# Optimization experiments

Hardware: AMD Instinct MI355X
Metric: run time of the kernel (lower is better)

Reference implementation:

```python
import jax, jax.numpy as jnp
import numpy as np

N, C, NE = 65536, 128, 10
INV_SQ2 = float(1.0 / np.sqrt(2.0))   # path weight sqrt(ir_out.dim / n_paths) * w3j, 0e outputs
INV_SQ6 = float(1.0 / np.sqrt(6.0))   # sqrt(1/2) * 1/sqrt(3) for the 1o.1o->0e dot path


def _fcn(x, weights):
    # e3nn FullyConnectedNet: no biases, fan-in normalized, silu between layers
    h = x
    for i, W in enumerate(weights):
        h = (h @ W) * float(1.0 / np.sqrt(W.shape[0]))
        if i < len(weights) - 1:
            h = jax.nn.silu(h)
    return h


def setup_inputs() -> dict:
    key = jax.random.key(0)
    ks = jax.random.split(key, 24)
    elem = jax.random.randint(ks[0], (N,), 0, NE)
    return {
        'node_feats_s': jax.random.normal(ks[1], (N, C), jnp.float32),
        'node_feats_v': jax.random.normal(ks[2], (N, C, 3), jnp.float32),
        'sc': jax.random.normal(ks[3], (N, 4 * C), jnp.float32),
        'node_attrs': jax.nn.one_hot(elem, NE, dtype=jnp.float32),
        'magmom_node_inv_feats': jax.random.normal(ks[4], (N, 16), jnp.float32),
        'magmom_node_attrs': jax.random.normal(ks[5], (N, 4), jnp.float32),
        'magmom_lenghts': jax.random.uniform(ks[6], (N, 1), jnp.float32),
        'Ws': jax.random.normal(ks[7], (NE, 5, C), jnp.float32),
        'Wv': jax.random.normal(ks[8], (NE, 4, C), jnp.float32),
        'Wc1': jax.random.normal(ks[9], (16, 64), jnp.float32),
        'Wc2': jax.random.normal(ks[10], (64, 64), jnp.float32),
        'Wc3': jax.random.normal(ks[11], (64, 64), jnp.float32),
        'Wc4': jax.random.normal(ks[12], (64, 4 * C), jnp.float32),
        'Wb1': jax.random.normal(ks[13], (16, 64), jnp.float32),
        'Wb2': jax.random.normal(ks[14], (64, 64), jnp.float32),
        'Wb3': jax.random.normal(ks[15], (64, 64), jnp.float32),
        'Wb4': jax.random.normal(ks[16], (64, C), jnp.float32),
        'exp_scaling': jnp.full((1,), 5.0, jnp.float32),
        'Wl0': jax.random.normal(ks[17], (2 * C, C), jnp.float32),
        'Wl1': jax.random.normal(ks[18], (2 * C, C), jnp.float32),
        'Wo0': jax.random.normal(ks[19], (C, C), jnp.float32),
        'Wo1': jax.random.normal(ks[20], (C, C), jnp.float32),
    }


def reference(node_feats_s, node_feats_v, sc, node_attrs, magmom_node_inv_feats,
              magmom_node_attrs, magmom_lenghts, Ws, Wv, Wc1, Wc2, Wc3, Wc4,
              Wb1, Wb2, Wb3, Wb4, exp_scaling, Wl0, Wl1, Wo0, Wo1):
    s, v = node_feats_s, node_feats_v                     # [N,C], [N,C,3]
    # --- SymmetricContraction (correlation 3, l<=1): per-element weighted symmetric CG basis ---
    ws = jnp.einsum('ne,epc->npc', node_attrs, Ws)        # [N,5,C] element-selected weights
    wv = jnp.einsum('ne,epc->npc', node_attrs, Wv)        # [N,4,C]
    vv = jnp.sum(v * v, axis=-1)                          # [N,C] invariant |v|^2
    out_s = (ws[:, 0] * s + ws[:, 1] * (s * s) + ws[:, 2] * vv
             + ws[:, 3] * (s * s * s) + ws[:, 4] * (s * vv))
    gate = wv[:, 0] + wv[:, 1] * s + wv[:, 2] * (s * s) + wv[:, 3] * vv
    out_v = gate[..., None] * v                           # [N,C,3] all 1o basis terms are multiples of v
    # --- conv_tp weights from invariant magmom feats ---
    tp_w = _fcn(magmom_node_inv_feats, [Wc1, Wc2, Wc3, Wc4])   # [N,4C]
    w0, w1, w2, w3 = (tp_w[:, 0:C], tp_w[:, C:2 * C], tp_w[:, 2 * C:3 * C], tp_w[:, 3 * C:4 * C])
    y0 = magmom_node_attrs[:, 0:1]                        # 1x0e
    y1 = magmom_node_attrs[:, 1:4]                        # 1x1o
    # --- path-sparse TensorProduct (uvu, per-sample weights), 4 instructions ---
    m0 = INV_SQ2 * w0 * out_s * y0                                     # 0e x 0e -> 0e
    m1 = INV_SQ6 * w1 * jnp.einsum('nci,ni->nc', out_v, y1)           # 1o x 1o -> 0e
    m2 = INV_SQ2 * w2[..., None] * out_s[..., None] * y1[:, None, :]  # 0e x 1o -> 1o
    m3 = INV_SQ2 * w3[..., None] * out_v * y0[:, :, None]             # 1o x 0e -> 1o
    # --- one-body magmom basis added to the scalar channels ---
    ob = _fcn(magmom_node_inv_feats, [Wb1, Wb2, Wb3, Wb4])            # [N,C]
    m0 = m0 + (1.0 - jnp.exp(-exp_scaling * magmom_lenghts)) * ob
    # --- equivariant Linear(irreps_mid -> target) + Linear(target -> target) + sc ---
    scal = jnp.concatenate([m0, m1], axis=1)              # [N,2C] 0e block
    vecs = jnp.concatenate([m2, m3], axis=1)              # [N,2C,3] 1o block
    inv_2c = float(1.0 / np.sqrt(2 * C))
    inv_c = float(1.0 / np.sqrt(C))
    out0 = (scal @ Wl0) * inv_2c
    out1 = jnp.einsum('nci,co->noi', vecs, Wl1) * inv_2c
    o0 = (out_s @ Wo0) * inv_c
    o1 = jnp.einsum('nci,co->noi', out_v, Wo1) * inv_c
    msg0 = out0 + o0 + sc[:, :C]
    msg1 = (out1 + o1).reshape(-1, 3 * C) + sc[:, C:]
    return jnp.concatenate([msg0, msg1], axis=1)          # [N, 4C] = target_irreps.dim
```

## Files before the change

kernel.cpp:

```cpp
#include <hip/hip_runtime.h>

#define NNODES 65536
#define CC 128
#define NEL 10
#define BN 32
#define NT 256

#define INV_SQ2f 0.70710678118654752440f
#define INV_SQ6f 0.40824829046386301637f
#define INV_2Cf  0.0625f
#define INV_Cf   0.08838834764831845f
#define S16f 0.25f
#define S64f 0.125f

#define WS_FRAGS 312
#define WS_BYTES (WS_FRAGS * 1024)

typedef __attribute__((ext_vector_type(8))) short s16x8;
typedef __attribute__((ext_vector_type(4))) float f32x4;
#define MFMA16(a, b, c) __builtin_amdgcn_mfma_f32_16x16x32_bf16((a), (b), (c), 0, 0, 0)

union U8 { unsigned short u[8]; s16x8 s; };

__device__ __forceinline__ unsigned short bf16rne(float x) {
    unsigned int u = __float_as_uint(x);
    return (unsigned short)((u + 0x7FFFu + ((u >> 16) & 1u)) >> 16);
}
__device__ __forceinline__ float bf2f(unsigned short h) {
    return __uint_as_float(((unsigned int)h) << 16);
}
__device__ __forceinline__ unsigned int packbf(float a, float b) {
    return (unsigned int)bf16rne(a) | (((unsigned int)bf16rne(b)) << 16);
}
__device__ __forceinline__ float siluf(float x) {
    return x * (1.0f / (1.0f + __expf(-x)));
}

extern "C" __global__ void prep_frags(
    const float* __restrict__ WC1, const float* __restrict__ WC2,
    const float* __restrict__ WC3, const float* __restrict__ WB1,
    const float* __restrict__ WB2, const float* __restrict__ WB3,
    const float* __restrict__ WC4, const float* __restrict__ WB4,
    const float* __restrict__ WL0, const float* __restrict__ WO0,
    const float* __restrict__ WL1, const float* __restrict__ WO1,
    unsigned short* __restrict__ wsb)
{
    const int b = blockIdx.x;
    const int l = threadIdx.x;
    const float* W; int K, N, nKS, base; float sc;
    if      (b <  4) { W = WC1; K = 16;  N = 64;  nKS = 1; base = 0;   sc = S16f; }
    else if (b < 12) { W = WC2; K = 64;  N = 64;  nKS = 2; base = 4;   sc = S64f; }
    else if (b < 20) { W = WC3; K = 64;  N = 64;  nKS = 2; base = 12;  sc = S64f; }
    else if (b < 24) { W = WB1; K = 16;  N = 64;  nKS = 1; base = 20;  sc = S16f; }
    else if (b < 32) { W = WB2; K = 64;  N = 64;  nKS = 2; base = 24;  sc = S64f; }
    else if (b < 40) { W = WB3; K = 64;  N = 64;  nKS = 2; base = 32;  sc = S64f; }
    else if (b < 104){ W = WC4; K = 64;  N = 512; nKS = 2; base = 40;  sc = S64f; }
    else if (b < 120){ W = WB4; K = 64;  N = 128; nKS = 2; base = 104; sc = S64f; }
    else if (b < 184){ W = WL0; K = 256; N = 128; nKS = 8; base = 120; sc = INV_2Cf; }
    else if (b < 216){ W = WO0; K = 128; N = 128; nKS = 4; base = 184; sc = INV_Cf; }
    else if (b < 280){ W = WL1; K = 256; N = 128; nKS = 8; base = 216; sc = INV_2Cf; }
    else             { W = WO1; K = 128; N = 128; nKS = 4; base = 280; sc = INV_Cf; }
    const int f  = b - base;
    const int nt = f / nKS, ks = f % nKS;
    const int n  = nt * 16 + (l & 15);
    const int k0 = ks * 32 + (l >> 4) * 8;
    U8 v;
    #pragma unroll
    for (int j = 0; j < 8; ++j) {
        const int k = k0 + j;
        const float x = (k < K) ? W[(size_t)k * N + n] * sc : 0.0f;
        v.u[j] = bf16rne(x);
    }
    *(s16x8*)(wsb + (size_t)b * 512 + l * 8) = v.s;
}

__device__ __forceinline__ s16x8 ldB(const unsigned short* __restrict__ wsb, int fragidx, int lane) {
    return *(const s16x8*)(wsb + ((size_t)fragidx << 9) + lane * 8);
}
__device__ __forceinline__ s16x8 ldA136(const unsigned short* X, int row, int ks, int gq) {
    return *(const s16x8*)(X + row * 136 + ks * 32 + gq * 8);
}
__device__ __forceinline__ s16x8 ldA72(const unsigned short* X, int row, int ks, int gq) {
    return *(const s16x8*)(X + row * 72 + ks * 32 + gq * 8);
}

extern "C" __global__ void __launch_bounds__(NT)
epb_mfma(const float* __restrict__ Sin, const float* __restrict__ Vin,
         const float* __restrict__ SCp, const float* __restrict__ ATT,
         const float* __restrict__ INVF, const float* __restrict__ MNA,
         const float* __restrict__ MLEN, const float* __restrict__ WSp,
         const float* __restrict__ WVp, const float* __restrict__ ESC,
         const unsigned short* __restrict__ wsb, float* __restrict__ OUT)
{
    extern __shared__ char smem[];
    unsigned short* B1 = (unsigned short*)smem;
    unsigned short* B2 = B1 + 4352;
    unsigned short* B3 = B2 + 4352;
    unsigned short* B4 = B3 + 4352;
    unsigned short* B5 = B4 + 4352;
    unsigned short* B6 = B5 + 4352;
    float* y0f  = (float*)(smem + 6 * 8704);
    float* y1f  = y0f + 32;
    float* etf  = y1f + 96;
    int*   eidx = (int*)(etf + 32);

    const int tid  = threadIdx.x;
    const int n0   = blockIdx.x * BN;
    const int w    = tid >> 6;
    const int lane = tid & 63;
    const int cl   = lane & 15;
    const int gq   = lane >> 4;
    const f32x4 Z4 = {0.f, 0.f, 0.f, 0.f};

    U8 invu[2];
    #pragma unroll
    for (int rg = 0; rg < 2; ++rg) {
        if (gq < 2) {
            const float* ip = INVF + (size_t)(n0 + rg * 16 + cl) * 16 + gq * 8;
            #pragma unroll
            for (int j = 0; j < 8; ++j) invu[rg].u[j] = bf16rne(ip[j]);
        } else {
            #pragma unroll
            for (int j = 0; j < 8; ++j) invu[rg].u[j] = 0;
        }
    }

    if (tid < BN) {
        const int gn = n0 + tid;
        y0f[tid] = MNA[gn * 4 + 0];
        y1f[tid * 3 + 0] = MNA[gn * 4 + 1];
        y1f[tid * 3 + 1] = MNA[gn * 4 + 2];
        y1f[tid * 3 + 2] = MNA[gn * 4 + 3];
        etf[tid] = 1.0f - __expf(-ESC[0] * MLEN[gn]);
        int e = 0;
        #pragma unroll
        for (int k = 0; k < NEL; ++k)
            if (ATT[(size_t)gn * NEL + k] > 0.5f) e = k;
        eidx[tid] = e;
    }

    #pragma unroll
    for (int rg = 0; rg < 2; ++rg) {
        const f32x4 c = MFMA16(invu[rg].s, ldB(wsb, 0 + w, lane), Z4);
        const f32x4 b = MFMA16(invu[rg].s, ldB(wsb, 20 + w, lane), Z4);
        #pragma unroll
        for (int r = 0; r < 4; ++r) {
            const int rw = rg * 16 + gq * 4 + r;
            B1[rw * 72 + w * 16 + cl] = bf16rne(siluf(c[r]));
            B2[rw * 72 + w * 16 + cl] = bf16rne(siluf(b[r]));
        }
    }
    __syncthreads();

    {
        f32x4 c[2] = {Z4, Z4}, b[2] = {Z4, Z4};
        #pragma unroll
        for (int ks = 0; ks < 2; ++ks) {
            const s16x8 fc = ldB(wsb, 4 + w * 2 + ks, lane);
            const s16x8 fb = ldB(wsb, 24 + w * 2 + ks, lane);
            #pragma unroll
            for (int rg = 0; rg < 2; ++rg) {
                c[rg] = MFMA16(ldA72(B1, rg * 16 + cl, ks, gq), fc, c[rg]);
                b[rg] = MFMA16(ldA72(B2, rg * 16 + cl, ks, gq), fb, b[rg]);
            }
        }
        #pragma unroll
        for (int rg = 0; rg < 2; ++rg)
            #pragma unroll
            for (int r = 0; r < 4; ++r) {
                const int rw = rg * 16 + gq * 4 + r;
                B3[rw * 72 + w * 16 + cl] = bf16rne(siluf(c[rg][r]));
                B4[rw * 72 + w * 16 + cl] = bf16rne(siluf(b[rg][r]));
            }
    }
    __syncthreads();

    {
        f32x4 c[2] = {Z4, Z4}, b[2] = {Z4, Z4};
        #pragma unroll
        for (int ks = 0; ks < 2; ++ks) {
            const s16x8 fc = ldB(wsb, 12 + w * 2 + ks, lane);
            const s16x8 fb = ldB(wsb, 32 + w * 2 + ks, lane);
            #pragma unroll
            for (int rg = 0; rg < 2; ++rg) {
                c[rg] = MFMA16(ldA72(B3, rg * 16 + cl, ks, gq), fc, c[rg]);
                b[rg] = MFMA16(ldA72(B4, rg * 16 + cl, ks, gq), fb, b[rg]);
            }
        }
        #pragma unroll
        for (int rg = 0; rg < 2; ++rg)
            #pragma unroll
            for (int r = 0; r < 4; ++r) {
                const int rw = rg * 16 + gq * 4 + r;
                B5[rw * 72 + w * 16 + cl] = bf16rne(siluf(c[rg][r]));
                B6[rw * 72 + w * 16 + cl] = bf16rne(siluf(b[rg][r]));
            }
    }
    __syncthreads();

    s16x8 h3c[2][2], h3b[2][2];
    #pragma unroll
    for (int rg = 0; rg < 2; ++rg)
        #pragma unroll
        for (int ks = 0; ks < 2; ++ks) {
            h3c[rg][ks] = ldA72(B5, rg * 16 + cl, ks, gq);
            h3b[rg][ks] = ldA72(B6, rg * 16 + cl, ks, gq);
        }
    f32x4 obacc[2][2];
    #pragma unroll
    for (int tc = 0; tc < 2; ++tc) {
        const int T = w * 2 + tc;
        const s16x8 f0 = ldB(wsb, 104 + T * 2 + 0, lane);
        const s16x8 f1 = ldB(wsb, 104 + T * 2 + 1, lane);
        #pragma unroll
        for (int rg = 0; rg < 2; ++rg)
            obacc[rg][tc] = MFMA16(h3b[rg][1], f1, MFMA16(h3b[rg][0], f0, Z4));
    }

    unsigned int vpack[3][8];
    {
        const int row = tid >> 3;
        const int c0  = (tid & 7) << 4;
        const size_t gn = (size_t)(n0 + row);
        const float4 mna = *(const float4*)(MNA + gn * 4);
        const float y10 = mna.y, y11 = mna.z, y12 = mna.w;
        int e = 0;
        #pragma unroll
        for (int k = 0; k < NEL; ++k)
            if (ATT[gn * NEL + k] > 0.5f) e = k;
        const float* sp  = Sin + gn * CC + c0;
        const float* vp  = Vin + (gn * CC + c0) * 3;
        const float* wsp = WSp + ((size_t)e * 5) * CC + c0;
        const float* wvp = WVp + ((size_t)e * 4) * CC + c0;
        unsigned int* B1d = (unsigned int*)B1;
        unsigned int* B2d = (unsigned int*)B2;
        unsigned int* B3d = (unsigned int*)B3;
        const int dbase = row * 68 + (c0 >> 1);
        #pragma unroll
        for (int jp = 0; jp < 8; ++jp) {
            const int c = 2 * jp;
            const float2 s2 = *(const float2*)(sp + c);
            const float2 va = *(const float2*)(vp + 3 * c);
            const float2 vb = *(const float2*)(vp + 3 * c + 2);
            const float2 vc = *(const float2*)(vp + 3 * c + 4);
            vpack[0][jp] = packbf(va.x, vb.y);
            vpack[1][jp] = packbf(va.y, vc.x);
            vpack[2][jp] = packbf(vb.x, vc.y);
            const float vv0 = va.x * va.x + va.y * va.y + vb.x * vb.x;
            const float vv1 = vb.y * vb.y + vc.x * vc.x + vc.y * vc.y;
            const float vy0 = va.x * y10 + va.y * y11 + vb.x * y12;
            const float vy1 = vb.y * y10 + vc.x * y11 + vc.y * y12;
            const float2 p0 = *(const float2*)(wsp + 0 * CC + c);
            const float2 p1 = *(const float2*)(wsp + 1 * CC + c);
            const float2 p2 = *(const float2*)(wsp + 2 * CC + c);
            const float2 p3 = *(const float2*)(wsp + 3 * CC + c);
            const float2 p4 = *(const float2*)(wsp + 4 * CC + c);
            const float2 q0 = *(const float2*)(wvp + 0 * CC + c);
            const float2 q1 = *(const float2*)(wvp + 1 * CC + c);
            const float2 q2 = *(const float2*)(wvp + 2 * CC + c);
            const float2 q3 = *(const float2*)(wvp + 3 * CC + c);
            const float s0 = s2.x, s1 = s2.y;
            const float ss0 = s0 * s0, ss1 = s1 * s1;
            const float os0 = p0.x * s0 + p1.x * ss0 + p2.x * vv0 + p3.x * (ss0 * s0) + p4.x * (s0 * vv0);
            const float os1 = p0.y * s1 + p1.y * ss1 + p2.y * vv1 + p3.y * (ss1 * s1) + p4.y * (s1 * vv1);
            const float gt0 = q0.x + q1.x * s0 + q2.x * ss0 + q3.x * vv0;
            const float gt1 = q0.y + q1.y * s1 + q2.y * ss1 + q3.y * vv1;
            B1d[dbase + jp] = packbf(os0, os1);
            B2d[dbase + jp] = packbf(gt0, gt1);
            B3d[dbase + jp] = packbf(vy0, vy1);
        }
    }
    __syncthreads();

#define WCHUNK(q, wc)                                                          \
    {                                                                          \
        _Pragma("unroll")                                                      \
        for (int tc = 0; tc < 2; ++tc) {                                       \
            const int T = w * 2 + tc;                                          \
            const s16x8 f0 = ldB(wsb, 40 + ((q) * 8 + T) * 2 + 0, lane);       \
            const s16x8 f1 = ldB(wsb, 40 + ((q) * 8 + T) * 2 + 1, lane);       \
            _Pragma("unroll")                                                  \
            for (int rg = 0; rg < 2; ++rg)                                     \
                wc[rg][tc] = MFMA16(h3c[rg][1], f1, MFMA16(h3c[rg][0], f0, Z4)); \
        }                                                                      \
    }
    {
        f32x4 wc[2][2];
        WCHUNK(0, wc)
        #pragma unroll
        for (int rg = 0; rg < 2; ++rg)
            #pragma unroll
            for (int tc = 0; tc < 2; ++tc)
                #pragma unroll
                for (int r = 0; r < 4; ++r) {
                    const int rw = rg * 16 + gq * 4 + r;
                    const int col = (w * 2 + tc) * 16 + cl;
                    const float os = bf2f(B1[rw * 136 + col]);
                    B4[rw * 136 + col] = bf16rne(INV_SQ2f * wc[rg][tc][r] * os * y0f[rw]
                                                 + etf[rw] * obacc[rg][tc][r]);
                }
        WCHUNK(1, wc)
        #pragma unroll
        for (int rg = 0; rg < 2; ++rg)
            #pragma unroll
            for (int tc = 0; tc < 2; ++tc)
                #pragma unroll
                for (int r = 0; r < 4; ++r) {
                    const int rw = rg * 16 + gq * 4 + r;
                    const int col = (w * 2 + tc) * 16 + cl;
                    const float gt = bf2f(B2[rw * 136 + col]);
                    const float vy = bf2f(B3[rw * 136 + col]);
                    B3[rw * 136 + col] = bf16rne(INV_SQ6f * wc[rg][tc][r] * gt * vy);
                }
        WCHUNK(2, wc)
        #pragma unroll
        for (int rg = 0; rg < 2; ++rg)
            #pragma unroll
            for (int tc = 0; tc < 2; ++tc)
                #pragma unroll
                for (int r = 0; r < 4; ++r) {
                    const int rw = rg * 16 + gq * 4 + r;
                    const int col = (w * 2 + tc) * 16 + cl;
                    B6[rw * 136 + col] = bf16rne(INV_SQ2f * wc[rg][tc][r] * bf2f(B1[rw * 136 + col]));
                }
        WCHUNK(3, wc)
        #pragma unroll
        for (int rg = 0; rg < 2; ++rg)
            #pragma unroll
            for (int tc = 0; tc < 2; ++tc)
                #pragma unroll
                for (int r = 0; r < 4; ++r) {
                    const int rw = rg * 16 + gq * 4 + r;
                    const int col = (w * 2 + tc) * 16 + cl;
                    const float gt = bf2f(B2[rw * 136 + col]);
                    B5[rw * 136 + col] = bf16rne(INV_SQ2f * wc[rg][tc][r] * gt * y0f[rw]);
                }
    }
#undef WCHUNK
    __syncthreads();

    f32x4 tacc[2][2] = {{Z4, Z4}, {Z4, Z4}};
    {
        f32x4 acc[2][2] = {{Z4, Z4}, {Z4, Z4}};
        #pragma unroll
        for (int ks = 0; ks < 12; ++ks) {
            const unsigned short* Xa = (ks < 4) ? B4 : (ks < 8) ? B3 : B1;
            s16x8 a[2];
            #pragma unroll
            for (int rg = 0; rg < 2; ++rg) a[rg] = ldA136(Xa, rg * 16 + cl, ks & 3, gq);
            #pragma unroll
            for (int tc = 0; tc < 2; ++tc) {
                const int T = w * 2 + tc;
                const int fi = (ks < 8) ? (120 + T * 8 + ks) : (184 + T * 4 + (ks - 8));
                const s16x8 bfrag = ldB(wsb, fi, lane);
                #pragma unroll
                for (int rg = 0; rg < 2; ++rg)
                    acc[rg][tc] = MFMA16(a[rg], bfrag, acc[rg][tc]);
            }
        }
        #pragma unroll
        for (int ks = 0; ks < 4; ++ks) {
            s16x8 a[2];
            #pragma unroll
            for (int rg = 0; rg < 2; ++rg) a[rg] = ldA136(B6, rg * 16 + cl, ks, gq);
            #pragma unroll
            for (int tc = 0; tc < 2; ++tc) {
                const s16x8 bfrag = ldB(wsb, 216 + (w * 2 + tc) * 8 + ks, lane);
                #pragma unroll
                for (int rg = 0; rg < 2; ++rg)
                    tacc[rg][tc] = MFMA16(a[rg], bfrag, tacc[rg][tc]);
            }
        }
        #pragma unroll
        for (int rg = 0; rg < 2; ++rg)
            #pragma unroll
            for (int tc = 0; tc < 2; ++tc)
                #pragma unroll
                for (int r = 0; r < 4; ++r) {
                    const int rw = rg * 16 + gq * 4 + r;
                    const size_t o = (size_t)(n0 + rw) * 512 + (w * 2 + tc) * 16 + cl;
                    OUT[o] = acc[rg][tc][r] + SCp[o];
                }
    }
    __syncthreads();

    f32x4 acc3[3][2][2];

#define STAGE_I(i, DSTB, DSTG)                                                  \
    {                                                                           \
        const int dbase = (tid >> 3) * 68 + (tid & 7) * 8;                      \
        const unsigned int* bD = (const unsigned int*)B5;                       \
        const unsigned int* gD = (const unsigned int*)B2;                       \
        unsigned int* o1 = (unsigned int*)(DSTB);                               \
        unsigned int* o3 = (unsigned int*)(DSTG);                               \
        _Pragma("unroll")                                                       \
        for (int jp = 0; jp < 8; ++jp) {                                        \
            const unsigned int bd = bD[dbase + jp];                             \
            const unsigned int gd = gD[dbase + jp];                             \
            const float v0 = bf2f((unsigned short)(vpack[i][jp] & 0xffff));     \
            const float v1 = bf2f((unsigned short)(vpack[i][jp] >> 16));        \
            o1[dbase + jp] = packbf(bf2f((unsigned short)(bd & 0xffff)) * v0,   \
                                    bf2f((unsigned short)(bd >> 16)) * v1);     \
            o3[dbase + jp] = packbf(bf2f((unsigned short)(gd & 0xffff)) * v0,   \
                                    bf2f((unsigned short)(gd >> 16)) * v1);     \
        }                                                                       \
    }

#define GEMM_I(i, SRCB, SRCG)                                                   \
    {                                                                           \
        _Pragma("unroll")                                                       \
        for (int rg = 0; rg < 2; ++rg)                                          \
            _Pragma("unroll")                                                   \
            for (int tc = 0; tc < 2; ++tc) acc3[i][rg][tc] = Z4;                \
        _Pragma("unroll")                                                       \
        for (int ks = 0; ks < 4; ++ks) {                                        \
            s16x8 a1[2], a3[2];                                                 \
            _Pragma("unroll")                                                   \
            for (int rg = 0; rg < 2; ++rg) {                                    \
                a1[rg] = ldA136((SRCB), rg * 16 + cl, ks, gq);                  \
                a3[rg] = ldA136((SRCG), rg * 16 + cl, ks, gq);                  \
            }                                                                   \
            _Pragma("unroll")                                                   \
            for (int tc = 0; tc < 2; ++tc) {                                    \
                const int T = w * 2 + tc;                                       \
                const s16x8 fb = ldB(wsb, 216 + T * 8 + 4 + ks, lane);          \
                const s16x8 fg = ldB(wsb, 280 + T * 4 + ks, lane);              \
                _Pragma("unroll")                                               \
                for (int rg = 0; rg < 2; ++rg) {                                \
                    acc3[i][rg][tc] = MFMA16(a1[rg], fb, acc3[i][rg][tc]);      \
                    acc3[i][rg][tc] = MFMA16(a3[rg], fg, acc3[i][rg][tc]);      \
                }                                                               \
            }                                                                   \
        }                                                                       \
    }

    STAGE_I(0, B1, B3)
    __syncthreads();
    GEMM_I(0, B1, B3)
    STAGE_I(1, B4, B6)
    __syncthreads();
    GEMM_I(1, B4, B6)
    STAGE_I(2, B1, B3)
    __syncthreads();
    GEMM_I(2, B1, B3)

    #pragma unroll
    for (int rg = 0; rg < 2; ++rg)
        #pragma unroll
        for (int tc = 0; tc < 2; ++tc)
            #pragma unroll
            for (int r = 0; r < 4; ++r) {
                const int rw = rg * 16 + gq * 4 + r;
                const int col = (w * 2 + tc) * 16 + cl;
                const size_t o = (size_t)(n0 + rw) * 512 + 128 + (size_t)col * 3;
                const float tv = tacc[rg][tc][r];
                OUT[o + 0] = acc3[0][rg][tc][r] + tv * y1f[rw * 3 + 0] + SCp[o + 0];
                OUT[o + 1] = acc3[1][rg][tc][r] + tv * y1f[rw * 3 + 1] + SCp[o + 1];
                OUT[o + 2] = acc3[2][rg][tc][r] + tv * y1f[rw * 3 + 2] + SCp[o + 2];
            }
#undef STAGE_I
#undef GEMM_I
}

extern "C" void kernel_launch(void* const* d_in, const int* in_sizes, int n_in,
                              void* d_out, int out_size, void* d_ws, size_t ws_size,
                              hipStream_t stream)
{
    (void)in_sizes; (void)n_in; (void)out_size; (void)ws_size;
    const float* Sin  = (const float*)d_in[0];
    const float* Vin  = (const float*)d_in[1];
    const float* SCp  = (const float*)d_in[2];
    const float* ATT  = (const float*)d_in[3];
    const float* INVF = (const float*)d_in[4];
    const float* MNA  = (const float*)d_in[5];
    const float* MLEN = (const float*)d_in[6];
    const float* WSp  = (const float*)d_in[7];
    const float* WVp  = (const float*)d_in[8];
    const float* WC1  = (const float*)d_in[9];
    const float* WC2  = (const float*)d_in[10];
    const float* WC3  = (const float*)d_in[11];
    const float* WC4  = (const float*)d_in[12];
    const float* WB1  = (const float*)d_in[13];
    const float* WB2  = (const float*)d_in[14];
    const float* WB3  = (const float*)d_in[15];
    const float* WB4  = (const float*)d_in[16];
    const float* ESC  = (const float*)d_in[17];
    const float* WL0  = (const float*)d_in[18];
    const float* WL1  = (const float*)d_in[19];
    const float* WO0  = (const float*)d_in[20];
    const float* WO1  = (const float*)d_in[21];
    float* OUT = (float*)d_out;

    unsigned short* wsb = (unsigned short*)d_ws;
    hipLaunchKernelGGL(prep_frags, dim3(WS_FRAGS), dim3(64), 0, stream,
                       WC1, WC2, WC3, WB1, WB2, WB3, WC4, WB4,
                       WL0, WO0, WL1, WO1, wsb);
    const size_t shbytes = (size_t)(6 * 8704 + 768);
    hipLaunchKernelGGL(epb_mfma, dim3(NNODES / BN), dim3(NT), shbytes, stream,
                       Sin, Vin, SCp, ATT, INVF, MNA, MLEN, WSp, WVp, ESC,
                       wsb, OUT);
}
```

Baseline: 166.4 us.

## Double threads per block to 512, one output tile per wave

Raises the block size from 256 to 512 threads so each of the 8 waves owns a single 16-column output tile, and splits the two MLP chains across wave halves. This removes the per-wave tc loop and halves the per-thread staging work and accumulator registers, which should raise latency hiding and occupancy. In exchange each wave reloads the A fragments that used to be shared across two column tiles, which adds LDS traffic. The unused element-index precompute is also dropped.

```diff
diff --git a/kernel.cpp b/kernel.cpp
--- a/kernel.cpp
+++ b/kernel.cpp
@@ -4,7 +4,7 @@
 #define CC 128
 #define NEL 10
 #define BN 32
-#define NT 256
+#define NT 512
 
 #define INV_SQ2f 0.70710678118654752440f
 #define INV_SQ6f 0.40824829046386301637f
@@ -102,7 +102,6 @@
     float* y0f  = (float*)(smem + 6 * 8704);
     float* y1f  = y0f + 32;
     float* etf  = y1f + 96;
-    int*   eidx = (int*)(etf + 32);
 
     const int tid  = threadIdx.x;
     const int n0   = blockIdx.x * BN;
@@ -110,6 +109,9 @@
     const int lane = tid & 63;
     const int cl   = lane & 15;
     const int gq   = lane >> 4;
+    const int T    = w;
+    const int mch  = w >> 2;
+    const int mt   = w & 3;
     const f32x4 Z4 = {0.f, 0.f, 0.f, 0.f};
 
     U8 invu[2];
@@ -132,68 +134,63 @@
         y1f[tid * 3 + 1] = MNA[gn * 4 + 2];
         y1f[tid * 3 + 2] = MNA[gn * 4 + 3];
         etf[tid] = 1.0f - __expf(-ESC[0] * MLEN[gn]);
-        int e = 0;
-        #pragma unroll
-        for (int k = 0; k < NEL; ++k)
-            if (ATT[(size_t)gn * NEL + k] > 0.5f) e = k;
-        eidx[tid] = e;
-    }
-
-    #pragma unroll
-    for (int rg = 0; rg < 2; ++rg) {
-        const f32x4 c = MFMA16(invu[rg].s, ldB(wsb, 0 + w, lane), Z4);
-        const f32x4 b = MFMA16(invu[rg].s, ldB(wsb, 20 + w, lane), Z4);
-        #pragma unroll
-        for (int r = 0; r < 4; ++r) {
-            const int rw = rg * 16 + gq * 4 + r;
-            B1[rw * 72 + w * 16 + cl] = bf16rne(siluf(c[r]));
-            B2[rw * 72 + w * 16 + cl] = bf16rne(siluf(b[r]));
-        }
-    }
-    __syncthreads();
-
-    {
-        f32x4 c[2] = {Z4, Z4}, b[2] = {Z4, Z4};
+    }
+
+    {
+        unsigned short* Hd = mch ? B2 : B1;
+        const int fi = (mch ? 20 : 0) + mt;
+        #pragma unroll
+        for (int rg = 0; rg < 2; ++rg) {
+            const f32x4 c = MFMA16(invu[rg].s, ldB(wsb, fi, lane), Z4);
+            #pragma unroll
+            for (int r = 0; r < 4; ++r) {
+                const int rw = rg * 16 + gq * 4 + r;
+                Hd[rw * 72 + mt * 16 + cl] = bf16rne(siluf(c[r]));
+            }
+        }
+    }
+    __syncthreads();
+
+    {
+        const unsigned short* Hs = mch ? B2 : B1;
+        unsigned short* Hd = mch ? B4 : B3;
+        const int base = mch ? 24 : 4;
+        f32x4 c[2] = {Z4, Z4};
         #pragma unroll
         for (int ks = 0; ks < 2; ++ks) {
-            const s16x8 fc = ldB(wsb, 4 + w * 2 + ks, lane);
-            const s16x8 fb = ldB(wsb, 24 + w * 2 + ks, lane);
-            #pragma unroll
-            for (int rg = 0; rg < 2; ++rg) {
-                c[rg] = MFMA16(ldA72(B1, rg * 16 + cl, ks, gq), fc, c[rg]);
-                b[rg] = MFMA16(ldA72(B2, rg * 16 + cl, ks, gq), fb, b[rg]);
-            }
-        }
-        #pragma unroll
-        for (int rg = 0; rg < 2; ++rg)
-            #pragma unroll
-            for (int r = 0; r < 4; ++r) {
-                const int rw = rg * 16 + gq * 4 + r;
-                B3[rw * 72 + w * 16 + cl] = bf16rne(siluf(c[rg][r]));
-                B4[rw * 72 + w * 16 + cl] = bf16rne(siluf(b[rg][r]));
-            }
-    }
-    __syncthreads();
-
-    {
-        f32x4 c[2] = {Z4, Z4}, b[2] = {Z4, Z4};
+            const s16x8 f = ldB(wsb, base + mt * 2 + ks, lane);
+            #pragma unroll
+            for (int rg = 0; rg < 2; ++rg)
+                c[rg] = MFMA16(ldA72(Hs, rg * 16 + cl, ks, gq), f, c[rg]);
+        }
+        #pragma unroll
+        for (int rg = 0; rg < 2; ++rg)
+            #pragma unroll
+            for (int r = 0; r < 4; ++r) {
+                const int rw = rg * 16 + gq * 4 + r;
+                Hd[rw * 72 + mt * 16 + cl] = bf16rne(siluf(c[rg][r]));
+            }
+    }
+    __syncthreads();
+
+    {
+        const unsigned short* Hs = mch ? B4 : B3;
+        unsigned short* Hd = mch ? B6 : B5;
+        const int base = mch ? 32 : 12;
+        f32x4 c[2] = {Z4, Z4};
         #pragma unroll
         for (int ks = 0; ks < 2; ++ks) {
-            const s16x8 fc = ldB(wsb, 12 + w * 2 + ks, lane);
-            const s16x8 fb = ldB(wsb, 32 + w * 2 + ks, lane);
-            #pragma unroll
-            for (int rg = 0; rg < 2; ++rg) {
-                c[rg] = MFMA16(ldA72(B3, rg * 16 + cl, ks, gq), fc, c[rg]);
-                b[rg] = MFMA16(ldA72(B4, rg * 16 + cl, ks, gq), fb, b[rg]);
-            }
-        }
-        #pragma unroll
-        for (int rg = 0; rg < 2; ++rg)
-            #pragma unroll
-            for (int r = 0; r < 4; ++r) {
-                const int rw = rg * 16 + gq * 4 + r;
-                B5[rw * 72 + w * 16 + cl] = bf16rne(siluf(c[rg][r]));
-                B6[rw * 72 + w * 16 + cl] = bf16rne(siluf(b[rg][r]));
+            const s16x8 f = ldB(wsb, base + mt * 2 + ks, lane);
+            #pragma unroll
+            for (int rg = 0; rg < 2; ++rg)
+                c[rg] = MFMA16(ldA72(Hs, rg * 16 + cl, ks, gq), f, c[rg]);
+        }
+        #pragma unroll
+        for (int rg = 0; rg < 2; ++rg)
+            #pragma unroll
+            for (int r = 0; r < 4; ++r) {
+                const int rw = rg * 16 + gq * 4 + r;
+                Hd[rw * 72 + mt * 16 + cl] = bf16rne(siluf(c[rg][r]));
             }
     }
     __syncthreads();
@@ -206,21 +203,19 @@
             h3c[rg][ks] = ldA72(B5, rg * 16 + cl, ks, gq);
             h3b[rg][ks] = ldA72(B6, rg * 16 + cl, ks, gq);
         }
-    f32x4 obacc[2][2];
-    #pragma unroll
-    for (int tc = 0; tc < 2; ++tc) {
-        const int T = w * 2 + tc;
+    f32x4 obacc[2];
+    {
         const s16x8 f0 = ldB(wsb, 104 + T * 2 + 0, lane);
         const s16x8 f1 = ldB(wsb, 104 + T * 2 + 1, lane);
         #pragma unroll
         for (int rg = 0; rg < 2; ++rg)
-            obacc[rg][tc] = MFMA16(h3b[rg][1], f1, MFMA16(h3b[rg][0], f0, Z4));
-    }
-
-    unsigned int vpack[3][8];
-    {
-        const int row = tid >> 3;
-        const int c0  = (tid & 7) << 4;
+            obacc[rg] = MFMA16(h3b[rg][1], f1, MFMA16(h3b[rg][0], f0, Z4));
+    }
+
+    unsigned int vpack[3][4];
+    {
+        const int row = tid >> 4;
+        const int c0  = (tid & 15) << 3;
         const size_t gn = (size_t)(n0 + row);
         const float4 mna = *(const float4*)(MNA + gn * 4);
         const float y10 = mna.y, y11 = mna.z, y12 = mna.w;
@@ -237,7 +232,7 @@
         unsigned int* B3d = (unsigned int*)B3;
         const int dbase = row * 68 + (c0 >> 1);
         #pragma unroll
-        for (int jp = 0; jp < 8; ++jp) {
+        for (int jp = 0; jp < 4; ++jp) {
             const int c = 2 * jp;
             const float2 s2 = *(const float2*)(sp + c);
             const float2 va = *(const float2*)(vp + 3 * c);
@@ -274,127 +269,100 @@
 
 #define WCHUNK(q, wc)                                                          \
     {                                                                          \
+        const s16x8 f0 = ldB(wsb, 40 + ((q) * 8 + T) * 2 + 0, lane);           \
+        const s16x8 f1 = ldB(wsb, 40 + ((q) * 8 + T) * 2 + 1, lane);           \
         _Pragma("unroll")                                                      \
-        for (int tc = 0; tc < 2; ++tc) {                                       \
-            const int T = w * 2 + tc;                                          \
-            const s16x8 f0 = ldB(wsb, 40 + ((q) * 8 + T) * 2 + 0, lane);       \
-            const s16x8 f1 = ldB(wsb, 40 + ((q) * 8 + T) * 2 + 1, lane);       \
-            _Pragma("unroll")                                                  \
-            for (int rg = 0; rg < 2; ++rg)                                     \
-                wc[rg][tc] = MFMA16(h3c[rg][1], f1, MFMA16(h3c[rg][0], f0, Z4)); \
-        }                                                                      \
-    }
-    {
-        f32x4 wc[2][2];
+        for (int rg = 0; rg < 2; ++rg)                                         \
+            wc[rg] = MFMA16(h3c[rg][1], f1, MFMA16(h3c[rg][0], f0, Z4));       \
+    }
+    {
+        f32x4 wc[2];
         WCHUNK(0, wc)
         #pragma unroll
         for (int rg = 0; rg < 2; ++rg)
             #pragma unroll
-            for (int tc = 0; tc < 2; ++tc)
-                #pragma unroll
-                for (int r = 0; r < 4; ++r) {
-                    const int rw = rg * 16 + gq * 4 + r;
-                    const int col = (w * 2 + tc) * 16 + cl;
-                    const float os = bf2f(B1[rw * 136 + col]);
-                    B4[rw * 136 + col] = bf16rne(INV_SQ2f * wc[rg][tc][r] * os * y0f[rw]
-                                                 + etf[rw] * obacc[rg][tc][r]);
-                }
+            for (int r = 0; r < 4; ++r) {
+                const int rw = rg * 16 + gq * 4 + r;
+                const int col = T * 16 + cl;
+                const float os = bf2f(B1[rw * 136 + col]);
+                B4[rw * 136 + col] = bf16rne(INV_SQ2f * wc[rg][r] * os * y0f[rw]
+                                             + etf[rw] * obacc[rg][r]);
+            }
         WCHUNK(1, wc)
         #pragma unroll
         for (int rg = 0; rg < 2; ++rg)
             #pragma unroll
-            for (int tc = 0; tc < 2; ++tc)
-                #pragma unroll
-                for (int r = 0; r < 4; ++r) {
-                    const int rw = rg * 16 + gq * 4 + r;
-                    const int col = (w * 2 + tc) * 16 + cl;
-                    const float gt = bf2f(B2[rw * 136 + col]);
-                    const float vy = bf2f(B3[rw * 136 + col]);
-                    B3[rw * 136 + col] = bf16rne(INV_SQ6f * wc[rg][tc][r] * gt * vy);
-                }
+            for (int r = 0; r < 4; ++r) {
+                const int rw = rg * 16 + gq * 4 + r;
+                const int col = T * 16 + cl;
+                const float gt = bf2f(B2[rw * 136 + col]);
+                const float vy = bf2f(B3[rw * 136 + col]);
+                B3[rw * 136 + col] = bf16rne(INV_SQ6f * wc[rg][r] * gt * vy);
+            }
         WCHUNK(2, wc)
         #pragma unroll
         for (int rg = 0; rg < 2; ++rg)
             #pragma unroll
-            for (int tc = 0; tc < 2; ++tc)
-                #pragma unroll
-                for (int r = 0; r < 4; ++r) {
-                    const int rw = rg * 16 + gq * 4 + r;
-                    const int col = (w * 2 + tc) * 16 + cl;
-                    B6[rw * 136 + col] = bf16rne(INV_SQ2f * wc[rg][tc][r] * bf2f(B1[rw * 136 + col]));
-                }
+            for (int r = 0; r < 4; ++r) {
+                const int rw = rg * 16 + gq * 4 + r;
+                const int col = T * 16 + cl;
+                B6[rw * 136 + col] = bf16rne(INV_SQ2f * wc[rg][r] * bf2f(B1[rw * 136 + col]));
+            }
         WCHUNK(3, wc)
         #pragma unroll
         for (int rg = 0; rg < 2; ++rg)
             #pragma unroll
-            for (int tc = 0; tc < 2; ++tc)
-                #pragma unroll
-                for (int r = 0; r < 4; ++r) {
-                    const int rw = rg * 16 + gq * 4 + r;
-                    const int col = (w * 2 + tc) * 16 + cl;
-                    const float gt = bf2f(B2[rw * 136 + col]);
-                    B5[rw * 136 + col] = bf16rne(INV_SQ2f * wc[rg][tc][r] * gt * y0f[rw]);
-                }
+            for (int r = 0; r < 4; ++r) {
+                const int rw = rg * 16 + gq * 4 + r;
+                const int col = T * 16 + cl;
+                const float gt = bf2f(B2[rw * 136 + col]);
+                B5[rw * 136 + col] = bf16rne(INV_SQ2f * wc[rg][r] * gt * y0f[rw]);
+            }
     }
 #undef WCHUNK
     __syncthreads();
 
-    f32x4 tacc[2][2] = {{Z4, Z4}, {Z4, Z4}};
-    {
-        f32x4 acc[2][2] = {{Z4, Z4}, {Z4, Z4}};
+    f32x4 tacc[2] = {Z4, Z4};
+    {
+        f32x4 acc[2] = {Z4, Z4};
         #pragma unroll
         for (int ks = 0; ks < 12; ++ks) {
             const unsigned short* Xa = (ks < 4) ? B4 : (ks < 8) ? B3 : B1;
-            s16x8 a[2];
-            #pragma unroll
-            for (int rg = 0; rg < 2; ++rg) a[rg] = ldA136(Xa, rg * 16 + cl, ks & 3, gq);
-            #pragma unroll
-            for (int tc = 0; tc < 2; ++tc) {
-                const int T = w * 2 + tc;
-                const int fi = (ks < 8) ? (120 + T * 8 + ks) : (184 + T * 4 + (ks - 8));
-                const s16x8 bfrag = ldB(wsb, fi, lane);
-                #pragma unroll
-                for (int rg = 0; rg < 2; ++rg)
-                    acc[rg][tc] = MFMA16(a[rg], bfrag, acc[rg][tc]);
-            }
+            const int fi = (ks < 8) ? (120 + T * 8 + ks) : (184 + T * 4 + (ks - 8));
+            const s16x8 bfrag = ldB(wsb, fi, lane);
+            #pragma unroll
+            for (int rg = 0; rg < 2; ++rg)
+                acc[rg] = MFMA16(ldA136(Xa, rg * 16 + cl, ks & 3, gq), bfrag, acc[rg]);
         }
         #pragma unroll
         for (int ks = 0; ks < 4; ++ks) {
-            s16x8 a[2];
-            #pragma unroll
-            for (int rg = 0; rg < 2; ++rg) a[rg] = ldA136(B6, rg * 16 + cl, ks, gq);
-            #pragma unroll
-            for (int tc = 0; tc < 2; ++tc) {
-                const s16x8 bfrag = ldB(wsb, 216 + (w * 2 + tc) * 8 + ks, lane);
-                #pragma unroll
-                for (int rg = 0; rg < 2; ++rg)
-                    tacc[rg][tc] = MFMA16(a[rg], bfrag, tacc[rg][tc]);
-            }
-        }
-        #pragma unroll
-        for (int rg = 0; rg < 2; ++rg)
-            #pragma unroll
-            for (int tc = 0; tc < 2; ++tc)
-                #pragma unroll
-                for (int r = 0; r < 4; ++r) {
-                    const int rw = rg * 16 + gq * 4 + r;
-                    const size_t o = (size_t)(n0 + rw) * 512 + (w * 2 + tc) * 16 + cl;
-                    OUT[o] = acc[rg][tc][r] + SCp[o];
-                }
-    }
-    __syncthreads();
-
-    f32x4 acc3[3][2][2];
+            const s16x8 bfrag = ldB(wsb, 216 + T * 8 + ks, lane);
+            #pragma unroll
+            for (int rg = 0; rg < 2; ++rg)
+                tacc[rg] = MFMA16(ldA136(B6, rg * 16 + cl, ks, gq), bfrag, tacc[rg]);
+        }
+        #pragma unroll
+        for (int rg = 0; rg < 2; ++rg)
+            #pragma unroll
+            for (int r = 0; r < 4; ++r) {
+                const int rw = rg * 16 + gq * 4 + r;
+                const size_t o = (size_t)(n0 + rw) * 512 + T * 16 + cl;
+                OUT[o] = acc[rg][r] + SCp[o];
+            }
+    }
+    __syncthreads();
+
+    f32x4 acc3[3][2];
 
 #define STAGE_I(i, DSTB, DSTG)                                                  \
     {                                                                           \
-        const int dbase = (tid >> 3) * 68 + (tid & 7) * 8;                      \
+        const int dbase = (tid >> 4) * 68 + (tid & 15) * 4;                     \
         const unsigned int* bD = (const unsigned int*)B5;                       \
         const unsigned int* gD = (const unsigned int*)B2;                       \
         unsigned int* o1 = (unsigned int*)(DSTB);                               \
         unsigned int* o3 = (unsigned int*)(DSTG);                               \
         _Pragma("unroll")                                                       \
-        for (int jp = 0; jp < 8; ++jp) {                                        \
+        for (int jp = 0; jp < 4; ++jp) {                                        \
             const unsigned int bd = bD[dbase + jp];                             \
             const unsigned int gd = gD[dbase + jp];                             \
             const float v0 = bf2f((unsigned short)(vpack[i][jp] & 0xffff));     \
@@ -409,27 +377,15 @@
 #define GEMM_I(i, SRCB, SRCG)                                                   \
     {                                                                           \
         _Pragma("unroll")                                                       \
-        for (int rg = 0; rg < 2; ++rg)                                          \
-            _Pragma("unroll")                                                   \
-            for (int tc = 0; tc < 2; ++tc) acc3[i][rg][tc] = Z4;                \
+        for (int rg = 0; rg < 2; ++rg) acc3[i][rg] = Z4;                        \
         _Pragma("unroll")                                                       \
         for (int ks = 0; ks < 4; ++ks) {                                        \
-            s16x8 a1[2], a3[2];                                                 \
+            const s16x8 fb = ldB(wsb, 216 + T * 8 + 4 + ks, lane);              \
+            const s16x8 fg = ldB(wsb, 280 + T * 4 + ks, lane);                  \
             _Pragma("unroll")                                                   \
             for (int rg = 0; rg < 2; ++rg) {                                    \
-                a1[rg] = ldA136((SRCB), rg * 16 + cl, ks, gq);                  \
-                a3[rg] = ldA136((SRCG), rg * 16 + cl, ks, gq);                  \
-            }                                                                   \
-            _Pragma("unroll")                                                   \
-            for (int tc = 0; tc < 2; ++tc) {                                    \
-                const int T = w * 2 + tc;                                       \
-                const s16x8 fb = ldB(wsb, 216 + T * 8 + 4 + ks, lane);          \
-                const s16x8 fg = ldB(wsb, 280 + T * 4 + ks, lane);              \
-                _Pragma("unroll")                                               \
-                for (int rg = 0; rg < 2; ++rg) {                                \
-                    acc3[i][rg][tc] = MFMA16(a1[rg], fb, acc3[i][rg][tc]);      \
-                    acc3[i][rg][tc] = MFMA16(a3[rg], fg, acc3[i][rg][tc]);      \
-                }                                                               \
+                acc3[i][rg] = MFMA16(ldA136((SRCB), rg * 16 + cl, ks, gq), fb, acc3[i][rg]); \
+                acc3[i][rg] = MFMA16(ldA136((SRCG), rg * 16 + cl, ks, gq), fg, acc3[i][rg]); \
             }                                                                   \
         }                                                                       \
     }
@@ -447,17 +403,15 @@
     #pragma unroll
     for (int rg = 0; rg < 2; ++rg)
         #pragma unroll
-        for (int tc = 0; tc < 2; ++tc)
-            #pragma unroll
-            for (int r = 0; r < 4; ++r) {
-                const int rw = rg * 16 + gq * 4 + r;
-                const int col = (w * 2 + tc) * 16 + cl;
-                const size_t o = (size_t)(n0 + rw) * 512 + 128 + (size_t)col * 3;
-                const float tv = tacc[rg][tc][r];
-                OUT[o + 0] = acc3[0][rg][tc][r] + tv * y1f[rw * 3 + 0] + SCp[o + 0];
-                OUT[o + 1] = acc3[1][rg][tc][r] + tv * y1f[rw * 3 + 1] + SCp[o + 1];
-                OUT[o + 2] = acc3[2][rg][tc][r] + tv * y1f[rw * 3 + 2] + SCp[o + 2];
-            }
+        for (int r = 0; r < 4; ++r) {
+            const int rw = rg * 16 + gq * 4 + r;
+            const int col = T * 16 + cl;
+            const size_t o = (size_t)(n0 + rw) * 512 + 128 + (size_t)col * 3;
+            const float tv = tacc[rg][r];
+            OUT[o + 0] = acc3[0][rg][r] + tv * y1f[rw * 3 + 0] + SCp[o + 0];
+            OUT[o + 1] = acc3[1][rg][r] + tv * y1f[rw * 3 + 1] + SCp[o + 1];
+            OUT[o + 2] = acc3[2][rg][r] + tv * y1f[rw * 3 + 2] + SCp[o + 2];
+        }
 #undef STAGE_I
 #undef GEMM_I
 }
```

New measurement: 184.3 us. +10.8%, slower.
